# Kernel tuning notes

Hardware: AMD Instinct MI355X
Metric: run time of the kernel (lower is better)

Reference implementation:

```python
import jax, jax.numpy as jnp
import numpy as np

B, S, D, H = 4, 2048, 1024, 1024

def setup_inputs() -> dict:
    key = jax.random.key(0)
    ks = jax.random.split(key, 9)
    s_in = 1.0 / np.sqrt(D)
    s_h = 1.0 / np.sqrt(H)
    return {
        "x": jax.random.normal(ks[0], (B, S, D), dtype=jnp.float32),
        "Wq": jax.random.normal(ks[1], (D, H), dtype=jnp.float32) * s_in,
        "bq": jnp.zeros((H,), dtype=jnp.float32),
        "Wk": jax.random.normal(ks[2], (D, H), dtype=jnp.float32) * s_in,
        "bk": jnp.zeros((H,), dtype=jnp.float32),
        "Wv": jax.random.normal(ks[3], (D, H), dtype=jnp.float32) * s_in,
        "bv": jnp.zeros((H,), dtype=jnp.float32),
        "Wo": jax.random.normal(ks[4], (H, D), dtype=jnp.float32) * s_h,
        "bo": jnp.zeros((D,), dtype=jnp.float32),
    }

def reference(x, Wq, bq, Wk, bk, Wv, bv, Wo, bo):
    # q,k,v: [B,S,H]
    q = jnp.einsum("bsd,dh->bsh", x, Wq) + bq
    k = jnp.einsum("bsd,dh->bsh", x, Wk) + bk
    v = jnp.einsum("bsd,dh->bsh", x, Wv) + bv
    # NOTE: original module has NO 1/sqrt(d) scaling
    scores = jnp.einsum("bqh,bkh->bqk", q, k)  # [B,S,S]
    attn = jax.nn.softmax(scores, axis=-1)
    y = jnp.einsum("bqk,bkh->bqh", attn, v)
    return jnp.einsum("bsh,hd->bsd", y, Wo) + bo
```

## Files before the change

### kernel.cpp

```cpp
#include <hip/hip_runtime.h>

typedef _Float16 f16x8 __attribute__((ext_vector_type(8)));
typedef float f32x4 __attribute__((ext_vector_type(4)));

#define GLD16(gp, lp) __builtin_amdgcn_global_load_lds(                     \
    (const __attribute__((address_space(1))) void*)(gp),                    \
    (__attribute__((address_space(3))) void*)(lp), 16, 0, 0)

__device__ inline void xcd_swizzle(int& bx, int& by) {
    const int nwg = gridDim.x * gridDim.y;
    const int flat = blockIdx.y * gridDim.x + blockIdx.x;
    const int cpx = nwg >> 3;
    const int swz = (flat & 7) * cpx + (flat >> 3);
    bx = swz % gridDim.x;
    by = swz / gridDim.x;
}

template <int MODE>
__global__ __launch_bounds__(512, 2)
void gemm_pl(const _Float16* __restrict__ A, const _Float16* __restrict__ B,
             void* __restrict__ C, const float* __restrict__ bias,
             int K, int lda, int ldb, int ldc, size_t sA, size_t sB, size_t sC)
{
    __shared__ __align__(16) _Float16 lds[3][(128 + 256) * 32];
    const int tid = threadIdx.x, wave = tid >> 6, lane = tid & 63;
    const int z = blockIdx.z;
    int bx, by; xcd_swizzle(bx, by);
    const int m0 = by * 128, n0 = bx * 256;

    const int trow = tid >> 2;
    const int schunk = (tid & 3) ^ ((trow >> 1) & 3);
    const char* pA = (const char*)(A + (size_t)z * sA + (size_t)(m0 + trow) * lda) + schunk * 16;
    const char* pB = (const char*)(B + (size_t)z * sB + (size_t)(n0 + trow) * ldb) + schunk * 16;
    const size_t hB = (size_t)128 * ldb * 2;

    auto stage = [&](int bf) {
        char* dA = (char*)&lds[bf][0] + tid * 16;
        char* dB = (char*)&lds[bf][128 * 32] + tid * 16;
        GLD16(pA, dA);
        GLD16(pB, dB); GLD16(pB + hB, dB + 8192);
        pA += 64; pB += 64;
    };

    const int wr = (wave >> 2) * 64, wcol = (wave & 3) * 64;
    const int fr = lane & 15;
    const int ckq = ((lane >> 4) ^ ((fr >> 1) & 3)) * 8;
    const int nt = K >> 5;

    const f32x4 zero = {0.f, 0.f, 0.f, 0.f};
    f32x4 acc[4][4];
#pragma unroll
    for (int i = 0; i < 4; ++i)
#pragma unroll
        for (int j = 0; j < 4; ++j) acc[i][j] = zero;

    stage(0); stage(1);
    asm volatile("s_waitcnt vmcnt(3)" ::: "memory");
    __builtin_amdgcn_s_barrier();
    __builtin_amdgcn_sched_barrier(0);

    for (int t = 0; t < nt; ++t) {
        const int cur = t % 3;
        if (t + 2 < nt) stage((t + 2) % 3);
        const _Float16* bA = &lds[cur][0];
        const _Float16* bB = &lds[cur][128 * 32];
        f16x8 af[4], bf4[4];
#pragma unroll
        for (int i = 0; i < 4; ++i)
            af[i] = *(const f16x8*)(bA + (wr + i * 16 + fr) * 32 + ckq);
#pragma unroll
        for (int j = 0; j < 4; ++j)
            bf4[j] = *(const f16x8*)(bB + (wcol + j * 16 + fr) * 32 + ckq);
        __builtin_amdgcn_s_setprio(1);
#pragma unroll
        for (int i = 0; i < 4; ++i)
#pragma unroll
            for (int j = 0; j < 4; ++j)
                acc[i][j] = __builtin_amdgcn_mfma_f32_16x16x32_f16(af[i], bf4[j], acc[i][j], 0, 0, 0);
        __builtin_amdgcn_s_setprio(0);
        __builtin_amdgcn_sched_barrier(0);
        if (t + 2 < nt) { asm volatile("s_waitcnt vmcnt(3)" ::: "memory"); }
        else           { asm volatile("s_waitcnt vmcnt(0)" ::: "memory"); }
        __builtin_amdgcn_s_barrier();
        __builtin_amdgcn_sched_barrier(0);
    }

    const int r0 = (lane >> 4) * 4;
#pragma unroll
    for (int j = 0; j < 4; ++j) {
        const int col = n0 + wcol + j * 16 + fr;
        const float bv = bias ? bias[col] : 0.0f;
#pragma unroll
        for (int i = 0; i < 4; ++i) {
            const int row = m0 + wr + i * 16 + r0;
            if constexpr (MODE == 0) {
                float* p = (float*)C + (size_t)z * sC + (size_t)row * ldc + col;
                p[0]               = acc[i][j][0] + bv;
                p[(size_t)ldc]     = acc[i][j][1] + bv;
                p[(size_t)2 * ldc] = acc[i][j][2] + bv;
                p[(size_t)3 * ldc] = acc[i][j][3] + bv;
            } else if constexpr (MODE == 1) {
                _Float16* p = (_Float16*)C + (size_t)z * sC + (size_t)row * ldc + col;
                p[0]               = (_Float16)(acc[i][j][0] + bv);
                p[(size_t)ldc]     = (_Float16)(acc[i][j][1] + bv);
                p[(size_t)2 * ldc] = (_Float16)(acc[i][j][2] + bv);
                p[(size_t)3 * ldc] = (_Float16)(acc[i][j][3] + bv);
            } else {
                const int bb = row >> 11, s = row & 2047;
                _Float16* p = (_Float16*)C + (((size_t)(bb << 10) + col) << 11) + s;
                p[0] = (_Float16)(acc[i][j][0] + bv);
                p[1] = (_Float16)(acc[i][j][1] + bv);
                p[2] = (_Float16)(acc[i][j][2] + bv);
                p[3] = (_Float16)(acc[i][j][3] + bv);
            }
        }
    }
}

template <int MODE>
__global__ __launch_bounds__(512, 2)
void gemm_spa256(const _Float16* __restrict__ Ah, const _Float16* __restrict__ Al,
                 const _Float16* __restrict__ B,
                 void* __restrict__ Cm, _Float16* __restrict__ Ca,
                 const float* __restrict__ bias,
                 int K, int lda, int ldb, int ldc, int CaCols,
                 size_t sA, size_t sB, size_t sC)
{
    __shared__ __align__(16) _Float16 lds[3][3][256 * 32];
    const int tid = threadIdx.x, wave = tid >> 6, lane = tid & 63;
    const int z = blockIdx.z;
    int bx, by; xcd_swizzle(bx, by);
    const int m0 = by * 256, n0 = bx * 256;

    const int trow = tid >> 2;
    const int schunk = (tid & 3) ^ ((trow >> 1) & 3);
    const char* pAh = (const char*)(Ah + (size_t)z * sA + (size_t)(m0 + trow) * lda) + schunk * 16;
    const char* pAl = (const char*)(Al + (size_t)z * sA + (size_t)(m0 + trow) * lda) + schunk * 16;
    const char* pB  = (const char*)(B  + (size_t)z * sB + (size_t)(n0 + trow) * ldb) + schunk * 16;
    const size_t hA = (size_t)128 * lda * 2;
    const size_t hB = (size_t)128 * ldb * 2;

    auto stage = [&](int bf) {
        char* d0 = (char*)&lds[bf][0][0] + tid * 16;
        char* d1 = (char*)&lds[bf][1][0] + tid * 16;
        char* d2 = (char*)&lds[bf][2][0] + tid * 16;
        GLD16(pAh, d0); GLD16(pAh + hA, d0 + 8192);
        GLD16(pAl, d1); GLD16(pAl + hA, d1 + 8192);
        GLD16(pB,  d2); GLD16(pB  + hB, d2 + 8192);
        pAh += 64; pAl += 64; pB += 64;
    };

    const int wr = (wave >> 1) * 64, wcol = (wave & 1) * 128;
    const int fr = lane & 15;
    const int ckq = ((lane >> 4) ^ ((fr >> 1) & 3)) * 8;
    const int nt = K >> 5;

    const f32x4 zero = {0.f, 0.f, 0.f, 0.f};
    f32x4 acc[4][8];
#pragma unroll
    for (int i = 0; i < 4; ++i)
#pragma unroll
        for (int j = 0; j < 8; ++j) acc[i][j] = zero;

    stage(0); stage(1);
    asm volatile("s_waitcnt vmcnt(6)" ::: "memory");
    __builtin_amdgcn_s_barrier();
    __builtin_amdgcn_sched_barrier(0);

    for (int t = 0; t < nt; ++t) {
        const int cur = t % 3;
        if (t + 2 < nt) stage((t + 2) % 3);
        const _Float16* bAh = &lds[cur][0][0];
        const _Float16* bAl = &lds[cur][1][0];
        const _Float16* bB  = &lds[cur][2][0];
        f16x8 af[4], al4[4], bf8[8];
#pragma unroll
        for (int i = 0; i < 4; ++i) {
            af[i]  = *(const f16x8*)(bAh + (wr + i * 16 + fr) * 32 + ckq);
            al4[i] = *(const f16x8*)(bAl + (wr + i * 16 + fr) * 32 + ckq);
        }
#pragma unroll
        for (int j = 0; j < 8; ++j)
            bf8[j] = *(const f16x8*)(bB + (wcol + j * 16 + fr) * 32 + ckq);
        __builtin_amdgcn_s_setprio(1);
#pragma unroll
        for (int i = 0; i < 4; ++i)
#pragma unroll
            for (int j = 0; j < 8; ++j) {
                acc[i][j] = __builtin_amdgcn_mfma_f32_16x16x32_f16(af[i],  bf8[j], acc[i][j], 0, 0, 0);
                acc[i][j] = __builtin_amdgcn_mfma_f32_16x16x32_f16(al4[i], bf8[j], acc[i][j], 0, 0, 0);
            }
        __builtin_amdgcn_s_setprio(0);
        __builtin_amdgcn_sched_barrier(0);
        if (t + 2 < nt) { asm volatile("s_waitcnt vmcnt(6)" ::: "memory"); }
        else           { asm volatile("s_waitcnt vmcnt(0)" ::: "memory"); }
        __builtin_amdgcn_s_barrier();
        __builtin_amdgcn_sched_barrier(0);
    }

    const int r0 = (lane >> 4) * 4;
#pragma unroll
    for (int j = 0; j < 8; ++j) {
        const int col = n0 + wcol + j * 16 + fr;
        const float bv = (MODE == 1 && bias) ? bias[col] : 0.0f;
#pragma unroll
        for (int i = 0; i < 4; ++i) {
            const int row = m0 + wr + i * 16 + r0;
#pragma unroll
            for (int r = 0; r < 4; ++r) {
                const float val = acc[i][j][r] + bv;
                const size_t idx = (size_t)z * sC + (size_t)(row + r) * ldc + col;
                if constexpr (MODE == 0) {
                    ((float*)Cm)[idx] = val;
                } else {
                    const _Float16 hv = (_Float16)val;
                    ((_Float16*)Cm)[idx] = hv;
                    if (col < CaCols) Ca[idx] = (_Float16)(val - (float)hv);
                }
            }
        }
    }
}

template <int MODE>
__global__ __launch_bounds__(512, 2)
void gemm_nt256(const _Float16* __restrict__ A, const _Float16* __restrict__ B,
                void* __restrict__ Cm, _Float16* __restrict__ Ca,
                const float* __restrict__ bias,
                int K, int lda, int ldb, int ldc, int CaCols,
                size_t sA, size_t sB, size_t sC)
{
    __shared__ __align__(16) _Float16 lds[3][2][256 * 32];
    const int tid = threadIdx.x, wave = tid >> 6, lane = tid & 63;
    const int z = blockIdx.z;
    int bx, by; xcd_swizzle(bx, by);
    const int m0 = by * 256, n0 = bx * 256;

    const int trow = tid >> 2;
    const int schunk = (tid & 3) ^ ((trow >> 1) & 3);
    const char* pA = (const char*)(A + (size_t)z * sA + (size_t)(m0 + trow) * lda) + schunk * 16;
    const char* pB = (const char*)(B + (size_t)z * sB + (size_t)(n0 + trow) * ldb) + schunk * 16;
    const size_t hA = (size_t)128 * lda * 2;
    const size_t hB = (size_t)128 * ldb * 2;

    auto stage = [&](int bf) {
        char* d0 = (char*)&lds[bf][0][0] + tid * 16;
        char* d1 = (char*)&lds[bf][1][0] + tid * 16;
        GLD16(pA, d0); GLD16(pA + hA, d0 + 8192);
        GLD16(pB, d1); GLD16(pB + hB, d1 + 8192);
        pA += 64; pB += 64;
    };

    const int wr = (wave >> 1) * 64, wcol = (wave & 1) * 128;
    const int fr = lane & 15;
    const int ckq = ((lane >> 4) ^ ((fr >> 1) & 3)) * 8;
    const int nt = K >> 5;

    const f32x4 zero = {0.f, 0.f, 0.f, 0.f};
    f32x4 acc[4][8];
#pragma unroll
    for (int i = 0; i < 4; ++i)
#pragma unroll
        for (int j = 0; j < 8; ++j) acc[i][j] = zero;

    stage(0); stage(1);
    asm volatile("s_waitcnt vmcnt(4)" ::: "memory");
    __builtin_amdgcn_s_barrier();
    __builtin_amdgcn_sched_barrier(0);

    for (int t = 0; t < nt; ++t) {
        const int cur = t % 3;
        if (t + 2 < nt) stage((t + 2) % 3);
        const _Float16* bA = &lds[cur][0][0];
        const _Float16* bB = &lds[cur][1][0];
        f16x8 af[4], bf8[8];
#pragma unroll
        for (int i = 0; i < 4; ++i)
            af[i] = *(const f16x8*)(bA + (wr + i * 16 + fr) * 32 + ckq);
#pragma unroll
        for (int j = 0; j < 8; ++j)
            bf8[j] = *(const f16x8*)(bB + (wcol + j * 16 + fr) * 32 + ckq);
        __builtin_amdgcn_s_setprio(1);
#pragma unroll
        for (int i = 0; i < 4; ++i)
#pragma unroll
            for (int j = 0; j < 8; ++j)
                acc[i][j] = __builtin_amdgcn_mfma_f32_16x16x32_f16(af[i], bf8[j], acc[i][j], 0, 0, 0);
        __builtin_amdgcn_s_setprio(0);
        __builtin_amdgcn_sched_barrier(0);
        if (t + 2 < nt) { asm volatile("s_waitcnt vmcnt(4)" ::: "memory"); }
        else           { asm volatile("s_waitcnt vmcnt(0)" ::: "memory"); }
        __builtin_amdgcn_s_barrier();
        __builtin_amdgcn_sched_barrier(0);
    }

    const int r0 = (lane >> 4) * 4;
#pragma unroll
    for (int j = 0; j < 8; ++j) {
        const int col = n0 + wcol + j * 16 + fr;
        const float bv = bias ? bias[col] : 0.0f;
#pragma unroll
        for (int i = 0; i < 4; ++i) {
            const int row = m0 + wr + i * 16 + r0;
#pragma unroll
            for (int r = 0; r < 4; ++r) {
                const float val = acc[i][j][r] + bv;
                const size_t idx = (size_t)z * sC + (size_t)(row + r) * ldc + col;
                const _Float16 hv = (_Float16)val;
                ((_Float16*)Cm)[idx] = hv;
                if (col < CaCols) Ca[idx] = (_Float16)(val - (float)hv);
            }
        }
    }
}

__global__ __launch_bounds__(256)
void cvt_split_f16(const float* __restrict__ in, _Float16* __restrict__ hi,
                   _Float16* __restrict__ lo, int n8)
{
    const int t = blockIdx.x * 256 + threadIdx.x;
    if (t >= n8) return;
    const float4* p = (const float4*)in + (size_t)t * 2;
    const float4 a = p[0], b = p[1];
    const float v[8] = {a.x, a.y, a.z, a.w, b.x, b.y, b.z, b.w};
    f16x8 h, l;
#pragma unroll
    for (int j = 0; j < 8; ++j) {
        const _Float16 hv = (_Float16)v[j];
        h[j] = hv;
        l[j] = (_Float16)(v[j] - (float)hv);
    }
    ((f16x8*)hi)[t] = h;
    if (lo) ((f16x8*)lo)[t] = l;
}

__global__ __launch_bounds__(256)
void transpose_f16(const float* __restrict__ W, _Float16* __restrict__ hiT,
                   int rows, int cols)
{
    __shared__ float t[32][33];
    const int c0 = blockIdx.x * 32, r0 = blockIdx.y * 32;
    const int tx = threadIdx.x & 31, ty = threadIdx.x >> 5;
#pragma unroll
    for (int r = ty; r < 32; r += 8)
        t[r][tx] = W[(size_t)(r0 + r) * cols + (c0 + tx)];
    __syncthreads();
#pragma unroll
    for (int r = ty; r < 32; r += 8)
        hiT[(size_t)(c0 + r) * rows + (r0 + tx)] = (_Float16)t[tx][r];
}

__global__ __launch_bounds__(256)
void concat_bias(const float* __restrict__ a, const float* __restrict__ b,
                 float* __restrict__ o)
{
    const int t = blockIdx.x * 256 + threadIdx.x;
    o[t] = (t < 1024) ? a[t] : b[t - 1024];
}

__global__ __launch_bounds__(256)
void softmax_rows(const float* __restrict__ S, _Float16* __restrict__ P)
{
    const int row = blockIdx.x;
    const float* s = S + (size_t)row * 2048 + threadIdx.x * 8;
    float v[8];
    const float4 a = *(const float4*)s;
    const float4 b = *(const float4*)(s + 4);
    v[0] = a.x; v[1] = a.y; v[2] = a.z; v[3] = a.w;
    v[4] = b.x; v[5] = b.y; v[6] = b.z; v[7] = b.w;
    float mx = v[0];
#pragma unroll
    for (int j = 1; j < 8; ++j) mx = fmaxf(mx, v[j]);
    for (int off = 32; off; off >>= 1) mx = fmaxf(mx, __shfl_xor(mx, off, 64));
    __shared__ float redm[4], reds[4];
    const int wv = threadIdx.x >> 6;
    if ((threadIdx.x & 63) == 0) redm[wv] = mx;
    __syncthreads();
    mx = fmaxf(fmaxf(redm[0], redm[1]), fmaxf(redm[2], redm[3]));
    float sum = 0.f;
#pragma unroll
    for (int j = 0; j < 8; ++j) { v[j] = expf(v[j] - mx); sum += v[j]; }
    for (int off = 32; off; off >>= 1) sum += __shfl_xor(sum, off, 64);
    if ((threadIdx.x & 63) == 0) reds[wv] = sum;
    __syncthreads();
    const float inv = 1.0f / (reds[0] + reds[1] + reds[2] + reds[3]);
    f16x8 o;
#pragma unroll
    for (int j = 0; j < 8; ++j) o[j] = (_Float16)(v[j] * inv);
    *(f16x8*)(P + (size_t)row * 2048 + threadIdx.x * 8) = o;
}

extern "C" void kernel_launch(void* const* d_in, const int* in_sizes, int n_in,
                              void* d_out, int out_size, void* d_ws, size_t ws_size,
                              hipStream_t stream)
{
    (void)in_sizes; (void)n_in; (void)out_size;
    const float* x  = (const float*)d_in[0];
    const float* Wq = (const float*)d_in[1];
    const float* bq = (const float*)d_in[2];
    const float* Wk = (const float*)d_in[3];
    const float* bk = (const float*)d_in[4];
    const float* Wv = (const float*)d_in[5];
    const float* bv = (const float*)d_in[6];
    const float* Wo = (const float*)d_in[7];
    const float* bo = (const float*)d_in[8];
    float* out = (float*)d_out;

    constexpr int S = 2048, D = 1024, H = 1024, NBATCH = 4;
    constexpr size_t M  = (size_t)NBATCH * S;
    constexpr size_t SH = (size_t)S * H;
    constexpr size_t SS = (size_t)S * S;
    constexpr size_t QK = (size_t)S * 2048;

    char* w = (char*)d_ws;
    size_t off = 0;
    auto alloc = [&](size_t bytes) -> char* {
        char* p = w + off;
        off += (bytes + 255) & ~(size_t)255;
        return p;
    };

    _Float16* xh   = (_Float16*)alloc(M * D * 2);
    _Float16* wqkT = (_Float16*)alloc((size_t)2 * D * H * 2);
    _Float16* wvh  = (_Float16*)alloc((size_t)D * H * 2);
    _Float16* woh  = (_Float16*)alloc((size_t)H * D * 2);
    float*    bqk  = (float*)alloc(2048 * 4);
    _Float16* qkh  = (_Float16*)alloc(M * 2048 * 2);
    _Float16* qkl  = (_Float16*)alloc(M * 2048 * 2);
    _Float16* vT   = (_Float16*)alloc(M * H * 2);
    _Float16* yh   = xh;

    int NB = 1;
    if (ws_size >= off + (size_t)4 * SS * 4 + (size_t)4 * SS * 2 + 1024) NB = 4;
    float*    sc = (float*)alloc((size_t)NB * SS * 4);
    _Float16* Ph = (_Float16*)alloc((size_t)NB * SS * 2);

    cvt_split_f16<<<dim3((unsigned)(M * D / 8 / 256)), 256, 0, stream>>>(
        x, xh, nullptr, (int)(M * D / 8));
    dim3 tg(H / 32, D / 32);
    transpose_f16<<<tg, 256, 0, stream>>>(Wq, wqkT, D, H);
    transpose_f16<<<tg, 256, 0, stream>>>(Wk, wqkT + (size_t)D * H, D, H);
    transpose_f16<<<tg, 256, 0, stream>>>(Wv, wvh, D, H);
    transpose_f16<<<tg, 256, 0, stream>>>(Wo, woh, H, D);
    concat_bias<<<dim3(8), 256, 0, stream>>>(bq, bk, bqk);

    gemm_nt256<1><<<dim3(2048 / 256, M / 256), 512, 0, stream>>>(
        xh, wqkT, qkh, qkl, bqk,
        D, D, D, 2048, 1024, 0, 0, 0);

    gemm_pl<2><<<dim3(H / 256, M / 128), 512, 0, stream>>>(
        xh, wvh, vT, bv, D, D, D, 0, 0, 0, 0);

    for (int b0 = 0; b0 < NBATCH; b0 += NB) {
        gemm_spa256<0><<<dim3(S / 256, S / 256, NB), 512, 0, stream>>>(
            qkh + (size_t)b0 * QK, qkl + (size_t)b0 * QK,
            qkh + (size_t)b0 * QK + 1024,
            sc, nullptr, nullptr,
            H, 2048, 2048, S, 0, QK, QK, SS);
        softmax_rows<<<dim3(NB * S), 256, 0, stream>>>(sc, Ph);
        gemm_pl<1><<<dim3(H / 256, S / 128, NB), 512, 0, stream>>>(
            Ph, vT + (size_t)b0 * SH, yh + (size_t)b0 * SH, nullptr,
            S, S, S, H, SS, SH, SH);
    }

    gemm_pl<0><<<dim3(D / 256, M / 128), 512, 0, stream>>>(
        yh, woh, out, bo, H, H, H, D, 0, 0, 0);
}
```

Before: 252.1 us.

## Interleave global prefetch and LDS reads with MFMA phases in GEMM main loops

Splits each K-step of the three GEMM kernels into phases that each load two B fragments from LDS, issue part of the next tile's global-to-LDS prefetch, then run a small MFMA batch, separated by barriers and lgkmcnt waits. This spreads memory instructions across the compute so they overlap with MFMA work instead of being issued in one burst. It also cuts register pressure by keeping only two B fragments live. The cost is several extra workgroup barriers per K-step, which can stall waves and reduce overlap between the two resident workgroups.

```diff
diff --git a/kernel.cpp b/kernel.cpp
--- a/kernel.cpp
+++ b/kernel.cpp
@@ -6,6 +6,11 @@
 #define GLD16(gp, lp) __builtin_amdgcn_global_load_lds(                     \
     (const __attribute__((address_space(1))) void*)(gp),                    \
     (__attribute__((address_space(3))) void*)(lp), 16, 0, 0)
+
+#define MFMA16(a, b, c) __builtin_amdgcn_mfma_f32_16x16x32_f16((a), (b), (c), 0, 0, 0)
+#define SBAR()  __builtin_amdgcn_s_barrier()
+#define SCHED() __builtin_amdgcn_sched_barrier(0)
+#define LGKM0() asm volatile("s_waitcnt lgkmcnt(0)" ::: "memory")
 
 __device__ inline void xcd_swizzle(int& bx, int& by) {
     const int nwg = gridDim.x * gridDim.y;
@@ -56,33 +61,48 @@
 
     stage(0); stage(1);
     asm volatile("s_waitcnt vmcnt(3)" ::: "memory");
-    __builtin_amdgcn_s_barrier();
-    __builtin_amdgcn_sched_barrier(0);
+    SBAR(); SCHED();
 
     for (int t = 0; t < nt; ++t) {
-        const int cur = t % 3;
-        if (t + 2 < nt) stage((t + 2) % 3);
+        const int cur = t % 3, nxt = (t + 2) % 3;
+        const bool pf = (t + 2) < nt;
         const _Float16* bA = &lds[cur][0];
         const _Float16* bB = &lds[cur][128 * 32];
-        f16x8 af[4], bf4[4];
+        char* dA = (char*)&lds[nxt][0] + tid * 16;
+        char* dB = (char*)&lds[nxt][128 * 32] + tid * 16;
+        f16x8 af[4], bfA, bfB;
+
 #pragma unroll
         for (int i = 0; i < 4; ++i)
             af[i] = *(const f16x8*)(bA + (wr + i * 16 + fr) * 32 + ckq);
-#pragma unroll
-        for (int j = 0; j < 4; ++j)
-            bf4[j] = *(const f16x8*)(bB + (wcol + j * 16 + fr) * 32 + ckq);
+        bfA = *(const f16x8*)(bB + (wcol + fr) * 32 + ckq);
+        bfB = *(const f16x8*)(bB + (wcol + 16 + fr) * 32 + ckq);
+        if (pf) { GLD16(pA, dA); pA += 64; }
+        SCHED(); SBAR(); LGKM0(); SCHED();
         __builtin_amdgcn_s_setprio(1);
 #pragma unroll
-        for (int i = 0; i < 4; ++i)
-#pragma unroll
-            for (int j = 0; j < 4; ++j)
-                acc[i][j] = __builtin_amdgcn_mfma_f32_16x16x32_f16(af[i], bf4[j], acc[i][j], 0, 0, 0);
+        for (int i = 0; i < 4; ++i) {
+            acc[i][0] = MFMA16(af[i], bfA, acc[i][0]);
+            acc[i][1] = MFMA16(af[i], bfB, acc[i][1]);
+        }
         __builtin_amdgcn_s_setprio(0);
-        __builtin_amdgcn_sched_barrier(0);
-        if (t + 2 < nt) { asm volatile("s_waitcnt vmcnt(3)" ::: "memory"); }
-        else           { asm volatile("s_waitcnt vmcnt(0)" ::: "memory"); }
-        __builtin_amdgcn_s_barrier();
-        __builtin_amdgcn_sched_barrier(0);
+        SCHED(); SBAR();
+
+        bfA = *(const f16x8*)(bB + (wcol + 32 + fr) * 32 + ckq);
+        bfB = *(const f16x8*)(bB + (wcol + 48 + fr) * 32 + ckq);
+        if (pf) { GLD16(pB, dB); GLD16(pB + hB, dB + 8192); pB += 64; }
+        SCHED(); SBAR(); LGKM0(); SCHED();
+        __builtin_amdgcn_s_setprio(1);
+#pragma unroll
+        for (int i = 0; i < 4; ++i) {
+            acc[i][2] = MFMA16(af[i], bfA, acc[i][2]);
+            acc[i][3] = MFMA16(af[i], bfB, acc[i][3]);
+        }
+        __builtin_amdgcn_s_setprio(0);
+        SCHED();
+        if (pf) { asm volatile("s_waitcnt vmcnt(3)" ::: "memory"); }
+        else    { asm volatile("s_waitcnt vmcnt(0)" ::: "memory"); }
+        SBAR(); SCHED();
     }
 
     const int r0 = (lane >> 4) * 4;
@@ -164,38 +184,63 @@
 
     stage(0); stage(1);
     asm volatile("s_waitcnt vmcnt(6)" ::: "memory");
-    __builtin_amdgcn_s_barrier();
-    __builtin_amdgcn_sched_barrier(0);
+    SBAR(); SCHED();
 
     for (int t = 0; t < nt; ++t) {
-        const int cur = t % 3;
-        if (t + 2 < nt) stage((t + 2) % 3);
+        const int cur = t % 3, nxt = (t + 2) % 3;
+        const bool pf = (t + 2) < nt;
         const _Float16* bAh = &lds[cur][0][0];
         const _Float16* bAl = &lds[cur][1][0];
         const _Float16* bB  = &lds[cur][2][0];
-        f16x8 af[4], al4[4], bf8[8];
+        char* d0 = (char*)&lds[nxt][0][0] + tid * 16;
+        char* d1 = (char*)&lds[nxt][1][0] + tid * 16;
+        char* d2 = (char*)&lds[nxt][2][0] + tid * 16;
+        f16x8 af[4], al4[4], bfA, bfB;
+
 #pragma unroll
         for (int i = 0; i < 4; ++i) {
             af[i]  = *(const f16x8*)(bAh + (wr + i * 16 + fr) * 32 + ckq);
             al4[i] = *(const f16x8*)(bAl + (wr + i * 16 + fr) * 32 + ckq);
         }
-#pragma unroll
-        for (int j = 0; j < 8; ++j)
-            bf8[j] = *(const f16x8*)(bB + (wcol + j * 16 + fr) * 32 + ckq);
+        bfA = *(const f16x8*)(bB + (wcol + fr) * 32 + ckq);
+        bfB = *(const f16x8*)(bB + (wcol + 16 + fr) * 32 + ckq);
+        if (pf) { GLD16(pAh, d0); GLD16(pAh + hA, d0 + 8192); pAh += 64; }
+        SCHED(); SBAR(); LGKM0(); SCHED();
         __builtin_amdgcn_s_setprio(1);
 #pragma unroll
-        for (int i = 0; i < 4; ++i)
-#pragma unroll
-            for (int j = 0; j < 8; ++j) {
-                acc[i][j] = __builtin_amdgcn_mfma_f32_16x16x32_f16(af[i],  bf8[j], acc[i][j], 0, 0, 0);
-                acc[i][j] = __builtin_amdgcn_mfma_f32_16x16x32_f16(al4[i], bf8[j], acc[i][j], 0, 0, 0);
-            }
+        for (int i = 0; i < 4; ++i) {
+            acc[i][0] = MFMA16(af[i],  bfA, acc[i][0]);
+            acc[i][0] = MFMA16(al4[i], bfA, acc[i][0]);
+            acc[i][1] = MFMA16(af[i],  bfB, acc[i][1]);
+            acc[i][1] = MFMA16(al4[i], bfB, acc[i][1]);
+        }
         __builtin_amdgcn_s_setprio(0);
-        __builtin_amdgcn_sched_barrier(0);
-        if (t + 2 < nt) { asm volatile("s_waitcnt vmcnt(6)" ::: "memory"); }
-        else           { asm volatile("s_waitcnt vmcnt(0)" ::: "memory"); }
-        __builtin_amdgcn_s_barrier();
-        __builtin_amdgcn_sched_barrier(0);
+        SCHED(); SBAR();
+
+#pragma unroll
+        for (int p = 1; p < 4; ++p) {
+            bfA = *(const f16x8*)(bB + (wcol + (2 * p) * 16 + fr) * 32 + ckq);
+            bfB = *(const f16x8*)(bB + (wcol + (2 * p + 1) * 16 + fr) * 32 + ckq);
+            if (pf && p == 1) { GLD16(pAl, d1); GLD16(pAl + hA, d1 + 8192); pAl += 64; }
+            if (pf && p == 2) { GLD16(pB,  d2); GLD16(pB  + hB, d2 + 8192); pB  += 64; }
+            SCHED(); SBAR(); LGKM0(); SCHED();
+            __builtin_amdgcn_s_setprio(1);
+#pragma unroll
+            for (int i = 0; i < 4; ++i) {
+                acc[i][2 * p]     = MFMA16(af[i],  bfA, acc[i][2 * p]);
+                acc[i][2 * p]     = MFMA16(al4[i], bfA, acc[i][2 * p]);
+                acc[i][2 * p + 1] = MFMA16(af[i],  bfB, acc[i][2 * p + 1]);
+                acc[i][2 * p + 1] = MFMA16(al4[i], bfB, acc[i][2 * p + 1]);
+            }
+            __builtin_amdgcn_s_setprio(0);
+            SCHED();
+            if (p == 3) {
+                if (pf) { asm volatile("s_waitcnt vmcnt(6)" ::: "memory"); }
+                else    { asm volatile("s_waitcnt vmcnt(0)" ::: "memory"); }
+            }
+            SBAR();
+        }
+        SCHED();
     }
 
     const int r0 = (lane >> 4) * 4;
@@ -265,33 +310,54 @@
 
     stage(0); stage(1);
     asm volatile("s_waitcnt vmcnt(4)" ::: "memory");
-    __builtin_amdgcn_s_barrier();
-    __builtin_amdgcn_sched_barrier(0);
+    SBAR(); SCHED();
 
     for (int t = 0; t < nt; ++t) {
-        const int cur = t % 3;
-        if (t + 2 < nt) stage((t + 2) % 3);
+        const int cur = t % 3, nxt = (t + 2) % 3;
+        const bool pf = (t + 2) < nt;
         const _Float16* bA = &lds[cur][0][0];
         const _Float16* bB = &lds[cur][1][0];
-        f16x8 af[4], bf8[8];
+        char* d0 = (char*)&lds[nxt][0][0] + tid * 16;
+        char* d1 = (char*)&lds[nxt][1][0] + tid * 16;
+        f16x8 af[4], bfA, bfB;
+
 #pragma unroll
         for (int i = 0; i < 4; ++i)
             af[i] = *(const f16x8*)(bA + (wr + i * 16 + fr) * 32 + ckq);
-#pragma unroll
-        for (int j = 0; j < 8; ++j)
-            bf8[j] = *(const f16x8*)(bB + (wcol + j * 16 + fr) * 32 + ckq);
+        bfA = *(const f16x8*)(bB + (wcol + fr) * 32 + ckq);
+        bfB = *(const f16x8*)(bB + (wcol + 16 + fr) * 32 + ckq);
+        if (pf) { GLD16(pA, d0); GLD16(pA + hA, d0 + 8192); pA += 64; }
+        SCHED(); SBAR(); LGKM0(); SCHED();
         __builtin_amdgcn_s_setprio(1);
 #pragma unroll
-        for (int i = 0; i < 4; ++i)
-#pragma unroll
-            for (int j = 0; j < 8; ++j)
-                acc[i][j] = __builtin_amdgcn_mfma_f32_16x16x32_f16(af[i], bf8[j], acc[i][j], 0, 0, 0);
+        for (int i = 0; i < 4; ++i) {
+            acc[i][0] = MFMA16(af[i], bfA, acc[i][0]);
+            acc[i][1] = MFMA16(af[i], bfB, acc[i][1]);
+        }
         __builtin_amdgcn_s_setprio(0);
-        __builtin_amdgcn_sched_barrier(0);
-        if (t + 2 < nt) { asm volatile("s_waitcnt vmcnt(4)" ::: "memory"); }
-        else           { asm volatile("s_waitcnt vmcnt(0)" ::: "memory"); }
-        __builtin_amdgcn_s_barrier();
-        __builtin_amdgcn_sched_barrier(0);
+        SCHED(); SBAR();
+
+#pragma unroll
+        for (int p = 1; p < 4; ++p) {
+            bfA = *(const f16x8*)(bB + (wcol + (2 * p) * 16 + fr) * 32 + ckq);
+            bfB = *(const f16x8*)(bB + (wcol + (2 * p + 1) * 16 + fr) * 32 + ckq);
+            if (pf && p == 1) { GLD16(pB, d1); GLD16(pB + hB, d1 + 8192); pB += 64; }
+            SCHED(); SBAR(); LGKM0(); SCHED();
+            __builtin_amdgcn_s_setprio(1);
+#pragma unroll
+            for (int i = 0; i < 4; ++i) {
+                acc[i][2 * p]     = MFMA16(af[i], bfA, acc[i][2 * p]);
+                acc[i][2 * p + 1] = MFMA16(af[i], bfB, acc[i][2 * p + 1]);
+            }
+            __builtin_amdgcn_s_setprio(0);
+            SCHED();
+            if (p == 3) {
+                if (pf) { asm volatile("s_waitcnt vmcnt(4)" ::: "memory"); }
+                else    { asm volatile("s_waitcnt vmcnt(0)" ::: "memory"); }
+            }
+            SBAR();
+        }
+        SCHED();
     }
 
     const int r0 = (lane >> 4) * 4;
```

New measurement: 258.8 us. 1.03x slower.

## Prefetch next A fragments into registers and unroll GEMM loops by three

Applied to the files above, without the earlier changes.

All three GEMM kernels now unroll the K loop by the triple-buffer depth so LDS buffer indices become compile-time constants. Each step loads the A fragments for the next tile into registers while computing the current one, putting LDS reads in the shadow of the MFMAs. The waits before each barrier tighten from a partial vmcnt to vmcnt(0), which can expose global-load latency. Doubling the A fragment registers raises register pressure under the 2-waves-per-SIMD launch bound.

```diff
diff --git a/kernel.cpp b/kernel.cpp
--- a/kernel.cpp
+++ b/kernel.cpp
@@ -6,6 +6,11 @@
 #define GLD16(gp, lp) __builtin_amdgcn_global_load_lds(                     \
     (const __attribute__((address_space(1))) void*)(gp),                    \
     (__attribute__((address_space(3))) void*)(lp), 16, 0, 0)
+
+#define MFMA16(a, b, c) __builtin_amdgcn_mfma_f32_16x16x32_f16((a), (b), (c), 0, 0, 0)
+#define SBAR()  __builtin_amdgcn_s_barrier()
+#define SCHED() __builtin_amdgcn_sched_barrier(0)
+#define VM0()   asm volatile("s_waitcnt vmcnt(0)" ::: "memory")
 
 __device__ inline void xcd_swizzle(int& bx, int& by) {
     const int nwg = gridDim.x * gridDim.y;
@@ -34,9 +39,9 @@
     const char* pB = (const char*)(B + (size_t)z * sB + (size_t)(n0 + trow) * ldb) + schunk * 16;
     const size_t hB = (size_t)128 * ldb * 2;
 
-    auto stage = [&](int bf) {
-        char* dA = (char*)&lds[bf][0] + tid * 16;
-        char* dB = (char*)&lds[bf][128 * 32] + tid * 16;
+    auto stage = [&](int bf_) {
+        char* dA = (char*)&lds[bf_][0] + tid * 16;
+        char* dB = (char*)&lds[bf_][128 * 32] + tid * 16;
         GLD16(pA, dA);
         GLD16(pB, dB); GLD16(pB + hB, dB + 8192);
         pA += 64; pB += 64;
@@ -46,6 +51,7 @@
     const int fr = lane & 15;
     const int ckq = ((lane >> 4) ^ ((fr >> 1) & 3)) * 8;
     const int nt = K >> 5;
+    const int arow = (wr + fr) * 32 + ckq;
 
     const f32x4 zero = {0.f, 0.f, 0.f, 0.f};
     f32x4 acc[4][4];
@@ -54,35 +60,45 @@
 #pragma unroll
         for (int j = 0; j < 4; ++j) acc[i][j] = zero;
 
+    f16x8 ah[3][4];
+
     stage(0); stage(1);
-    asm volatile("s_waitcnt vmcnt(3)" ::: "memory");
-    __builtin_amdgcn_s_barrier();
-    __builtin_amdgcn_sched_barrier(0);
-
-    for (int t = 0; t < nt; ++t) {
-        const int cur = t % 3;
-        if (t + 2 < nt) stage((t + 2) % 3);
-        const _Float16* bA = &lds[cur][0];
-        const _Float16* bB = &lds[cur][128 * 32];
-        f16x8 af[4], bf4[4];
-#pragma unroll
-        for (int i = 0; i < 4; ++i)
-            af[i] = *(const f16x8*)(bA + (wr + i * 16 + fr) * 32 + ckq);
-#pragma unroll
-        for (int j = 0; j < 4; ++j)
-            bf4[j] = *(const f16x8*)(bB + (wcol + j * 16 + fr) * 32 + ckq);
-        __builtin_amdgcn_s_setprio(1);
-#pragma unroll
-        for (int i = 0; i < 4; ++i)
-#pragma unroll
-            for (int j = 0; j < 4; ++j)
-                acc[i][j] = __builtin_amdgcn_mfma_f32_16x16x32_f16(af[i], bf4[j], acc[i][j], 0, 0, 0);
-        __builtin_amdgcn_s_setprio(0);
-        __builtin_amdgcn_sched_barrier(0);
-        if (t + 2 < nt) { asm volatile("s_waitcnt vmcnt(3)" ::: "memory"); }
-        else           { asm volatile("s_waitcnt vmcnt(0)" ::: "memory"); }
-        __builtin_amdgcn_s_barrier();
-        __builtin_amdgcn_sched_barrier(0);
+    VM0(); SBAR(); SCHED();
+#pragma unroll
+    for (int i = 0; i < 4; ++i)
+        ah[0][i] = *(const f16x8*)(&lds[0][0] + arow + i * 512);
+
+    for (int tb = 0; tb < nt; tb += 3) {
+#pragma unroll
+        for (int u = 0; u < 3; ++u) {
+            const int t = tb + u;
+            if (t < nt) {
+                const int nx = (u + 1) % 3, st = (u + 2) % 3;
+                const _Float16* bB = &lds[u][128 * 32];
+                f16x8 bf[4];
+#pragma unroll
+                for (int j = 0; j < 4; ++j)
+                    bf[j] = *(const f16x8*)(bB + (wcol + j * 16 + fr) * 32 + ckq);
+                SCHED();
+                if (t + 2 < nt) stage(st);
+                if (t + 1 < nt) {
+#pragma unroll
+                    for (int i = 0; i < 4; ++i)
+                        ah[nx][i] = *(const f16x8*)(&lds[nx][0] + arow + i * 512);
+                }
+                SCHED();
+                __builtin_amdgcn_s_setprio(1);
+#pragma unroll
+                for (int j = 0; j < 4; ++j)
+#pragma unroll
+                    for (int i = 0; i < 4; ++i)
+                        acc[i][j] = MFMA16(ah[u][i], bf[j], acc[i][j]);
+                __builtin_amdgcn_s_setprio(0);
+                SCHED();
+                VM0();
+                SBAR(); SCHED();
+            }
+        }
     }
 
     const int r0 = (lane >> 4) * 4;
@@ -140,10 +156,10 @@
     const size_t hA = (size_t)128 * lda * 2;
     const size_t hB = (size_t)128 * ldb * 2;
 
-    auto stage = [&](int bf) {
-        char* d0 = (char*)&lds[bf][0][0] + tid * 16;
-        char* d1 = (char*)&lds[bf][1][0] + tid * 16;
-        char* d2 = (char*)&lds[bf][2][0] + tid * 16;
+    auto stage = [&](int bf_) {
+        char* d0 = (char*)&lds[bf_][0][0] + tid * 16;
+        char* d1 = (char*)&lds[bf_][1][0] + tid * 16;
+        char* d2 = (char*)&lds[bf_][2][0] + tid * 16;
         GLD16(pAh, d0); GLD16(pAh + hA, d0 + 8192);
         GLD16(pAl, d1); GLD16(pAl + hA, d1 + 8192);
         GLD16(pB,  d2); GLD16(pB  + hB, d2 + 8192);
@@ -154,6 +170,7 @@
     const int fr = lane & 15;
     const int ckq = ((lane >> 4) ^ ((fr >> 1) & 3)) * 8;
     const int nt = K >> 5;
+    const int arow = (wr + fr) * 32 + ckq;
 
     const f32x4 zero = {0.f, 0.f, 0.f, 0.f};
     f32x4 acc[4][8];
@@ -162,40 +179,51 @@
 #pragma unroll
         for (int j = 0; j < 8; ++j) acc[i][j] = zero;
 
+    f16x8 ah[3][4], al4[3][4];
+
     stage(0); stage(1);
-    asm volatile("s_waitcnt vmcnt(6)" ::: "memory");
-    __builtin_amdgcn_s_barrier();
-    __builtin_amdgcn_sched_barrier(0);
-
-    for (int t = 0; t < nt; ++t) {
-        const int cur = t % 3;
-        if (t + 2 < nt) stage((t + 2) % 3);
-        const _Float16* bAh = &lds[cur][0][0];
-        const _Float16* bAl = &lds[cur][1][0];
-        const _Float16* bB  = &lds[cur][2][0];
-        f16x8 af[4], al4[4], bf8[8];
-#pragma unroll
-        for (int i = 0; i < 4; ++i) {
-            af[i]  = *(const f16x8*)(bAh + (wr + i * 16 + fr) * 32 + ckq);
-            al4[i] = *(const f16x8*)(bAl + (wr + i * 16 + fr) * 32 + ckq);
+    VM0(); SBAR(); SCHED();
+#pragma unroll
+    for (int i = 0; i < 4; ++i) {
+        ah[0][i]  = *(const f16x8*)(&lds[0][0][0] + arow + i * 512);
+        al4[0][i] = *(const f16x8*)(&lds[0][1][0] + arow + i * 512);
+    }
+
+    for (int tb = 0; tb < nt; tb += 3) {
+#pragma unroll
+        for (int u = 0; u < 3; ++u) {
+            const int t = tb + u;
+            if (t < nt) {
+                const int nx = (u + 1) % 3, st = (u + 2) % 3;
+                const _Float16* bB = &lds[u][2][0];
+                f16x8 bf[8];
+#pragma unroll
+                for (int j = 0; j < 8; ++j)
+                    bf[j] = *(const f16x8*)(bB + (wcol + j * 16 + fr) * 32 + ckq);
+                SCHED();
+                if (t + 2 < nt) stage(st);
+                if (t + 1 < nt) {
+#pragma unroll
+                    for (int i = 0; i < 4; ++i) {
+                        ah[nx][i]  = *(const f16x8*)(&lds[nx][0][0] + arow + i * 512);
+                        al4[nx][i] = *(const f16x8*)(&lds[nx][1][0] + arow + i * 512);
+                    }
+                }
+                SCHED();
+                __builtin_amdgcn_s_setprio(1);
+#pragma unroll
+                for (int j = 0; j < 8; ++j)
+#pragma unroll
+                    for (int i = 0; i < 4; ++i) {
+                        acc[i][j] = MFMA16(ah[u][i],  bf[j], acc[i][j]);
+                        acc[i][j] = MFMA16(al4[u][i], bf[j], acc[i][j]);
+                    }
+                __builtin_amdgcn_s_setprio(0);
+                SCHED();
+                VM0();
+                SBAR(); SCHED();
+            }
         }
-#pragma unroll
-        for (int j = 0; j < 8; ++j)
-            bf8[j] = *(const f16x8*)(bB + (wcol + j * 16 + fr) * 32 + ckq);
-        __builtin_amdgcn_s_setprio(1);
-#pragma unroll
-        for (int i = 0; i < 4; ++i)
-#pragma unroll
-            for (int j = 0; j < 8; ++j) {
-                acc[i][j] = __builtin_amdgcn_mfma_f32_16x16x32_f16(af[i],  bf8[j], acc[i][j], 0, 0, 0);
-                acc[i][j] = __builtin_amdgcn_mfma_f32_16x16x32_f16(al4[i], bf8[j], acc[i][j], 0, 0, 0);
-            }
-        __builtin_amdgcn_s_setprio(0);
-        __builtin_amdgcn_sched_barrier(0);
-        if (t + 2 < nt) { asm volatile("s_waitcnt vmcnt(6)" ::: "memory"); }
-        else           { asm volatile("s_waitcnt vmcnt(0)" ::: "memory"); }
-        __builtin_amdgcn_s_barrier();
-        __builtin_amdgcn_sched_barrier(0);
     }
 
     const int r0 = (lane >> 4) * 4;
@@ -243,9 +271,9 @@
     const size_t hA = (size_t)128 * lda * 2;
     const size_t hB = (size_t)128 * ldb * 2;
 
-    auto stage = [&](int bf) {
-        char* d0 = (char*)&lds[bf][0][0] + tid * 16;
-        char* d1 = (char*)&lds[bf][1][0] + tid * 16;
+    auto stage = [&](int bf_) {
+        char* d0 = (char*)&lds[bf_][0][0] + tid * 16;
+        char* d1 = (char*)&lds[bf_][1][0] + tid * 16;
         GLD16(pA, d0); GLD16(pA + hA, d0 + 8192);
         GLD16(pB, d1); GLD16(pB + hB, d1 + 8192);
         pA += 64; pB += 64;
@@ -255,6 +283,7 @@
     const int fr = lane & 15;
     const int ckq = ((lane >> 4) ^ ((fr >> 1) & 3)) * 8;
     const int nt = K >> 5;
+    const int arow = (wr + fr) * 32 + ckq;
 
     const f32x4 zero = {0.f, 0.f, 0.f, 0.f};
     f32x4 acc[4][8];
@@ -263,35 +292,45 @@
 #pragma unroll
         for (int j = 0; j < 8; ++j) acc[i][j] = zero;
 
+    f16x8 ah[3][4];
+
     stage(0); stage(1);
-    asm volatile("s_waitcnt vmcnt(4)" ::: "memory");
-    __builtin_amdgcn_s_barrier();
-    __builtin_amdgcn_sched_barrier(0);
-
-    for (int t = 0; t < nt; ++t) {
-        const int cur = t % 3;
-        if (t + 2 < nt) stage((t + 2) % 3);
-        const _Float16* bA = &lds[cur][0][0];
-        const _Float16* bB = &lds[cur][1][0];
-        f16x8 af[4], bf8[8];
-#pragma unroll
-        for (int i = 0; i < 4; ++i)
-            af[i] = *(const f16x8*)(bA + (wr + i * 16 + fr) * 32 + ckq);
-#pragma unroll
-        for (int j = 0; j < 8; ++j)
-            bf8[j] = *(const f16x8*)(bB + (wcol + j * 16 + fr) * 32 + ckq);
-        __builtin_amdgcn_s_setprio(1);
-#pragma unroll
-        for (int i = 0; i < 4; ++i)
-#pragma unroll
-            for (int j = 0; j < 8; ++j)
-                acc[i][j] = __builtin_amdgcn_mfma_f32_16x16x32_f16(af[i], bf8[j], acc[i][j], 0, 0, 0);
-        __builtin_amdgcn_s_setprio(0);
-        __builtin_amdgcn_sched_barrier(0);
-        if (t + 2 < nt) { asm volatile("s_waitcnt vmcnt(4)" ::: "memory"); }
-        else           { asm volatile("s_waitcnt vmcnt(0)" ::: "memory"); }
-        __builtin_amdgcn_s_barrier();
-        __builtin_amdgcn_sched_barrier(0);
+    VM0(); SBAR(); SCHED();
+#pragma unroll
+    for (int i = 0; i < 4; ++i)
+        ah[0][i] = *(const f16x8*)(&lds[0][0][0] + arow + i * 512);
+
+    for (int tb = 0; tb < nt; tb += 3) {
+#pragma unroll
+        for (int u = 0; u < 3; ++u) {
+            const int t = tb + u;
+            if (t < nt) {
+                const int nx = (u + 1) % 3, st = (u + 2) % 3;
+                const _Float16* bB = &lds[u][1][0];
+                f16x8 bf[8];
+#pragma unroll
+                for (int j = 0; j < 8; ++j)
+                    bf[j] = *(const f16x8*)(bB + (wcol + j * 16 + fr) * 32 + ckq);
+                SCHED();
+                if (t + 2 < nt) stage(st);
+                if (t + 1 < nt) {
+#pragma unroll
+                    for (int i = 0; i < 4; ++i)
+                        ah[nx][i] = *(const f16x8*)(&lds[nx][0][0] + arow + i * 512);
+                }
+                SCHED();
+                __builtin_amdgcn_s_setprio(1);
+#pragma unroll
+                for (int j = 0; j < 8; ++j)
+#pragma unroll
+                    for (int i = 0; i < 4; ++i)
+                        acc[i][j] = MFMA16(ah[u][i], bf[j], acc[i][j]);
+                __builtin_amdgcn_s_setprio(0);
+                SCHED();
+                VM0();
+                SBAR(); SCHED();
+            }
+        }
     }
 
     const int r0 = (lane >> 4) * 4;
```

New measurement: 344.1 us. 36.5% more time.
